# Optimization experiments

Hardware: AMD Instinct MI355X
Metric: run time of the kernel (lower is better)

The kernel has to match this reference:

```python
import jax, jax.numpy as jnp
import numpy as np


def setup_inputs() -> dict:
    key = jax.random.key(0)
    k1, k2, k3, k4 = jax.random.split(key, 4)
    batch, seq, d_model = 4, 4096, 2048
    num_atoms, num_layers, rank = 64, 16, 6
    hidden = jax.random.normal(k1, (batch, seq, d_model), dtype=jnp.float32)
    atom_scales = jax.random.uniform(k2, (batch, num_atoms), dtype=jnp.float32)
    # q_proj atoms: proj_dim == d_model == 2048
    A = jax.random.normal(k3, (num_atoms, num_layers, d_model, rank), dtype=jnp.float32) * 0.01
    B = jax.random.normal(k4, (num_atoms, num_layers, rank, d_model), dtype=jnp.float32) * 0.01
    return {"hidden": hidden, "atom_scales": atom_scales, "A": A, "B": B, "layer_idx": 5}


def reference(hidden, atom_scales, A, B, layer_idx):
    # Select this layer's atom factors: (atoms, d_model, rank) / (atoms, rank, proj_dim)
    A_l = A[:, layer_idx]
    B_l = B[:, layer_idx]
    # Down-project into rank-6 per atom: (batch, atoms, seq, rank)
    projections = jnp.einsum('bsd,adr->basr', hidden, A_l)
    # Per-(batch, atom) scalar blend weights
    scaled = projections * atom_scales[:, :, None, None]
    # Up-project and sum over atoms: (batch, seq, proj_dim)
    lora_out = jnp.einsum('basr,arp->bsp', scaled, B_l)
    return lora_out
```

## Files before the change

kernel.cpp:

```cpp
#include <hip/hip_runtime.h>
#include <hip/hip_bf16.h>

typedef __attribute__((ext_vector_type(4))) float  f32x4;
typedef __attribute__((ext_vector_type(8))) short  s16x8;

#define D_MODEL 2048
#define SEQ     4096
#define BATCH   4
#define NATOMS  64
#define RANK    6
#define NLAYERS 16
#define NAR     (NATOMS*RANK)
#define M_TOTAL (BATCH*SEQ)

#define ASZ  (64*72)
#define WSZ  (384*64)
#define BSZ  (64*392)
#define PSTR 392

static __device__ __forceinline__ unsigned short f2bf(float x){
    union { float f; unsigned u; } v; v.f = x;
    unsigned r = (v.u + 0x7FFF + ((v.u >> 16) & 1)) >> 16;
    return (unsigned short)r;
}

static __device__ __forceinline__ void gload_lds16(const void* g, void* l) {
    __builtin_amdgcn_global_load_lds(
        (const __attribute__((address_space(1))) unsigned int*)g,
        (__attribute__((address_space(3))) unsigned int*)l, 16, 0, 0);
}

static __device__ __forceinline__ s16x8 cvt8(f32x4 lo, f32x4 hi) {
    union { s16x8 v; unsigned short s[8]; } u;
    u.s[0] = f2bf(lo.x); u.s[1] = f2bf(lo.y); u.s[2] = f2bf(lo.z); u.s[3] = f2bf(lo.w);
    u.s[4] = f2bf(hi.x); u.s[5] = f2bf(hi.y); u.s[6] = f2bf(hi.z); u.s[7] = f2bf(hi.w);
    return u.v;
}

__global__ void prep_kernel(const float* __restrict__ A,
                            const float* __restrict__ B,
                            const int*   __restrict__ layer_idx,
                            unsigned short* __restrict__ WbfT,
                            unsigned short* __restrict__ BbfT)
{
    const int l = layer_idx[0];
    int idx = blockIdx.x * 256 + threadIdx.x;
    const int total = NAR * D_MODEL;
    if (idx < total) {
        int n = idx / D_MODEL, d = idx % D_MODEL;
        int a = n / RANK, r = n % RANK;
        float v = A[((size_t)(a*NLAYERS + l) * D_MODEL + d) * RANK + r];
        WbfT[idx] = f2bf(v);
    } else {
        idx -= total;
        int p = idx / NAR, n = idx % NAR;
        int a = n / RANK, r = n % RANK;
        float v = B[((size_t)(a*NLAYERS + l) * RANK + r) * D_MODEL + p];
        BbfT[idx] = f2bf(v);
    }
}

__global__ __launch_bounds__(512, 1) void fused_lora(
    const float*          __restrict__ hidden,
    const float*          __restrict__ scales,
    const unsigned short* __restrict__ WbfT,
    const unsigned short* __restrict__ BbfT,
    float*                __restrict__ out)
{
    __shared__ __align__(16) char smem[150528];
    unsigned short* Af = (unsigned short*)smem;
    unsigned short* Wf = (unsigned short*)(smem + 18432);
    unsigned short* Pl = (unsigned short*)smem;
    unsigned short* Bt = (unsigned short*)(smem + 50176);

    const int m0   = blockIdx.x * 64;
    const int tid  = threadIdx.x;
    const int lane = tid & 63;
    const int w    = tid >> 6;
    const int wr   = w >> 2, wc = w & 3;

    const int rowA = tid >> 3;
    const int c8A  = tid & 7;
    const float* srcA = hidden + (size_t)(m0 + rowA) * D_MODEL + c8A * 8;

    const unsigned short* srcW[6];
    int ldsW[6];
    #pragma unroll
    for (int j = 0; j < 6; ++j) {
        int i = w * 6 + j;
        int r = i * 8 + (lane >> 3);
        int c = (lane & 7) ^ (r & 7);
        srcW[j] = WbfT + (size_t)r * D_MODEL + c * 8;
        ldsW[j] = i * 512;
    }

    f32x4 acc[2][6] = {};
    f32x4 ga[2], gb[2];

    ga[0] = *reinterpret_cast<const f32x4*>(srcA);
    ga[1] = *reinterpret_cast<const f32x4*>(srcA + 4);
    srcA += 64;
    {
        s16x8 s = cvt8(ga[0], ga[1]);
        *reinterpret_cast<s16x8*>(&Af[rowA * 72 + c8A * 8]) = s;
    }
    #pragma unroll
    for (int j = 0; j < 6; ++j) { gload_lds16(srcW[j], &Wf[ldsW[j]]); srcW[j] += 64; }
    __builtin_amdgcn_sched_barrier(0);
    gb[0] = *reinterpret_cast<const f32x4*>(srcA);
    gb[1] = *reinterpret_cast<const f32x4*>(srcA + 4);
    srcA += 64;
    asm volatile("s_waitcnt vmcnt(2) lgkmcnt(0)" ::: "memory");
    __builtin_amdgcn_s_barrier();

    auto body = [&](int t, f32x4 (&gI)[2], f32x4 (&gC)[2]) {
        const int buf = t & 1;
        if (t < 31) {
            #pragma unroll
            for (int j = 0; j < 6; ++j) {
                gload_lds16(srcW[j], &Wf[(buf ^ 1) * WSZ + ldsW[j]]);
                srcW[j] += 64;
            }
        }
        __builtin_amdgcn_sched_barrier(0);
        if (t < 30) {
            gI[0] = *reinterpret_cast<const f32x4*>(srcA);
            gI[1] = *reinterpret_cast<const f32x4*>(srcA + 4);
            srcA += 64;
        }
        const unsigned short* Ar = &Af[buf * ASZ];
        const unsigned short* Wr = &Wf[buf * WSZ];
        #pragma unroll
        for (int kk = 0; kk < 2; ++kk) {
            const int kch = kk * 4 + (lane >> 4);
            s16x8 bfr[6], afr[2];
            #pragma unroll
            for (int ni = 0; ni < 6; ++ni) {
                int br = wc * 96 + ni * 16 + (lane & 15);
                bfr[ni] = *reinterpret_cast<const s16x8*>(
                    &Wr[br * 64 + ((kch ^ (br & 7)) << 3)]);
            }
            #pragma unroll
            for (int mi = 0; mi < 2; ++mi) {
                int ar = wr * 32 + mi * 16 + (lane & 15);
                afr[mi] = *reinterpret_cast<const s16x8*>(
                    &Ar[ar * 72 + kk * 32 + (lane >> 4) * 8]);
            }
            #pragma unroll
            for (int mi = 0; mi < 2; ++mi)
                #pragma unroll
                for (int ni = 0; ni < 6; ++ni)
                    acc[mi][ni] = __builtin_amdgcn_mfma_f32_16x16x32_bf16(
                        afr[mi], bfr[ni], acc[mi][ni], 0, 0, 0);
        }
        if (t < 31) {
            s16x8 s = cvt8(gC[0], gC[1]);
            *reinterpret_cast<s16x8*>(&Af[(buf ^ 1) * ASZ + rowA * 72 + c8A * 8]) = s;
            if (t == 30) asm volatile("s_waitcnt vmcnt(0) lgkmcnt(0)" ::: "memory");
            else         asm volatile("s_waitcnt vmcnt(2) lgkmcnt(0)" ::: "memory");
            __builtin_amdgcn_s_barrier();
        }
    };
    for (int tt = 0; tt < 32; tt += 2) {
        body(tt,     ga, gb);
        body(tt + 1, gb, ga);
    }
    __syncthreads();

    const int b = m0 >> 12;
    #pragma unroll
    for (int ni = 0; ni < 6; ++ni) {
        int col  = wc * 96 + ni * 16 + (lane & 15);
        float sc = scales[b * NATOMS + col / RANK];
        #pragma unroll
        for (int mi = 0; mi < 2; ++mi) {
            #pragma unroll
            for (int r = 0; r < 4; ++r) {
                int row = wr * 32 + mi * 16 + (lane >> 4) * 4 + r;
                Pl[row * PSTR + col] = f2bf(acc[mi][ni][r] * sc);
            }
        }
    }
    __syncthreads();

    const int wr2 = w >> 2, wp = w & 3;
    const unsigned short* srcB[6];
    int dstB[6];
    #pragma unroll
    for (int j = 0; j < 6; ++j) {
        int g  = j * 512 + tid;
        int rB = g / 48, cB = g % 48;
        srcB[j] = BbfT + (size_t)rB * NAR + cB * 8;
        dstB[j] = rB * PSTR + cB * 8;
    }
    s16x8 pf[2][12];
    #pragma unroll
    for (int mi = 0; mi < 2; ++mi)
        #pragma unroll
        for (int ks = 0; ks < 12; ++ks)
            pf[mi][ks] = *reinterpret_cast<const s16x8*>(
                &Pl[(wr2 * 32 + mi * 16 + (lane & 15)) * PSTR + (ks * 4 + (lane >> 4)) * 8]);

    s16x8 gB[6];
    #pragma unroll
    for (int j = 0; j < 6; ++j) gB[j] = *reinterpret_cast<const s16x8*>(srcB[j]);
    #pragma unroll
    for (int j = 0; j < 6; ++j) *reinterpret_cast<s16x8*>(&Bt[dstB[j]]) = gB[j];
    asm volatile("s_waitcnt lgkmcnt(0)" ::: "memory");
    __builtin_amdgcn_s_barrier();

    for (int pt = 0; pt < 32; ++pt) {
        const int buf = pt & 1;
        if (pt < 31) {
            #pragma unroll
            for (int j = 0; j < 6; ++j)
                gB[j] = *reinterpret_cast<const s16x8*>(srcB[j] + (size_t)(pt + 1) * 64 * NAR);
        }
        f32x4 a2[2] = {};
        #pragma unroll
        for (int ks = 0; ks < 12; ++ks) {
            s16x8 bfr = *reinterpret_cast<const s16x8*>(
                &Bt[buf * BSZ + (wp * 16 + (lane & 15)) * PSTR + (ks * 4 + (lane >> 4)) * 8]);
            #pragma unroll
            for (int mi = 0; mi < 2; ++mi)
                a2[mi] = __builtin_amdgcn_mfma_f32_16x16x32_bf16(
                    pf[mi][ks], bfr, a2[mi], 0, 0, 0);
        }
        #pragma unroll
        for (int mi = 0; mi < 2; ++mi) {
            #pragma unroll
            for (int r = 0; r < 4; ++r) {
                int row = m0 + wr2 * 32 + mi * 16 + (lane >> 4) * 4 + r;
                int col = pt * 64 + wp * 16 + (lane & 15);
                out[(size_t)row * D_MODEL + col] = a2[mi][r];
            }
        }
        if (pt < 31) {
            #pragma unroll
            for (int j = 0; j < 6; ++j)
                *reinterpret_cast<s16x8*>(&Bt[(buf ^ 1) * BSZ + dstB[j]]) = gB[j];
            asm volatile("s_waitcnt lgkmcnt(0)" ::: "memory");
            __builtin_amdgcn_s_barrier();
        }
    }
}

extern "C" void kernel_launch(void* const* d_in, const int* in_sizes, int n_in,
                              void* d_out, int out_size, void* d_ws, size_t ws_size,
                              hipStream_t stream)
{
    const float* hidden    = (const float*)d_in[0];
    const float* scales    = (const float*)d_in[1];
    const float* A         = (const float*)d_in[2];
    const float* B         = (const float*)d_in[3];
    const int*   layer_idx = (const int*)d_in[4];
    float* out = (float*)d_out;

    unsigned short* WbfT = (unsigned short*)d_ws;
    unsigned short* BbfT = WbfT + (size_t)NAR * D_MODEL;

    prep_kernel<<<(2 * NAR * D_MODEL) / 256, 256, 0, stream>>>(A, B, layer_idx, WbfT, BbfT);
    fused_lora<<<M_TOTAL / 64, 512, 0, stream>>>(hidden, scales, WbfT, BbfT, out);
}
```

Before: 93.97 us.

## Load up-projection B fragments directly into registers instead of staging through LDS

The second GEMM phase no longer copies B tiles into a double-buffered LDS area behind barriers. Each wave now loads its own B fragments from global memory straight into registers, double-buffered in a ping-pong loop, and re-reads the P fragments from LDS every iteration instead of keeping them in registers. This drops the per-tile barriers and LDS writes and shrinks the shared memory allocation. The cost is redundant global loads of B across the two row-waves, which should mostly hit L2, plus more LDS reads for P.

```diff
diff --git a/kernel.cpp b/kernel.cpp
--- a/kernel.cpp
+++ b/kernel.cpp
@@ -15,7 +15,6 @@
 
 #define ASZ  (64*72)
 #define WSZ  (384*64)
-#define BSZ  (64*392)
 #define PSTR 392
 
 static __device__ __forceinline__ unsigned short f2bf(float x){
@@ -67,11 +66,10 @@
     const unsigned short* __restrict__ BbfT,
     float*                __restrict__ out)
 {
-    __shared__ __align__(16) char smem[150528];
+    __shared__ __align__(16) char smem[116736];
     unsigned short* Af = (unsigned short*)smem;
     unsigned short* Wf = (unsigned short*)(smem + 18432);
     unsigned short* Pl = (unsigned short*)smem;
-    unsigned short* Bt = (unsigned short*)(smem + 50176);
 
     const int m0   = blockIdx.x * 64;
     const int tid  = threadIdx.x;
@@ -184,47 +182,31 @@
     __syncthreads();
 
     const int wr2 = w >> 2, wp = w & 3;
-    const unsigned short* srcB[6];
-    int dstB[6];
-    #pragma unroll
-    for (int j = 0; j < 6; ++j) {
-        int g  = j * 512 + tid;
-        int rB = g / 48, cB = g % 48;
-        srcB[j] = BbfT + (size_t)rB * NAR + cB * 8;
-        dstB[j] = rB * PSTR + cB * 8;
-    }
-    s16x8 pf[2][12];
-    #pragma unroll
-    for (int mi = 0; mi < 2; ++mi)
-        #pragma unroll
-        for (int ks = 0; ks < 12; ++ks)
-            pf[mi][ks] = *reinterpret_cast<const s16x8*>(
-                &Pl[(wr2 * 32 + mi * 16 + (lane & 15)) * PSTR + (ks * 4 + (lane >> 4)) * 8]);
-
-    s16x8 gB[6];
-    #pragma unroll
-    for (int j = 0; j < 6; ++j) gB[j] = *reinterpret_cast<const s16x8*>(srcB[j]);
-    #pragma unroll
-    for (int j = 0; j < 6; ++j) *reinterpret_cast<s16x8*>(&Bt[dstB[j]]) = gB[j];
-    asm volatile("s_waitcnt lgkmcnt(0)" ::: "memory");
-    __builtin_amdgcn_s_barrier();
-
-    for (int pt = 0; pt < 32; ++pt) {
-        const int buf = pt & 1;
+    const unsigned short* srcB2 =
+        BbfT + (size_t)(wp * 16 + (lane & 15)) * NAR + (lane >> 4) * 8;
+    const unsigned short* PlBase = &Pl[(wr2 * 32 + (lane & 15)) * PSTR + (lane >> 4) * 8];
+
+    s16x8 bA[12], bB[12];
+    #pragma unroll
+    for (int ks = 0; ks < 12; ++ks)
+        bA[ks] = *reinterpret_cast<const s16x8*>(srcB2 + ks * 32);
+
+    auto p2body = [&](int pt, s16x8 (&bC)[12], s16x8 (&bN)[12]) {
         if (pt < 31) {
-            #pragma unroll
-            for (int j = 0; j < 6; ++j)
-                gB[j] = *reinterpret_cast<const s16x8*>(srcB[j] + (size_t)(pt + 1) * 64 * NAR);
+            const unsigned short* s2 = srcB2 + (size_t)(pt + 1) * 64 * NAR;
+            #pragma unroll
+            for (int ks = 0; ks < 12; ++ks)
+                bN[ks] = *reinterpret_cast<const s16x8*>(s2 + ks * 32);
         }
         f32x4 a2[2] = {};
         #pragma unroll
         for (int ks = 0; ks < 12; ++ks) {
-            s16x8 bfr = *reinterpret_cast<const s16x8*>(
-                &Bt[buf * BSZ + (wp * 16 + (lane & 15)) * PSTR + (ks * 4 + (lane >> 4)) * 8]);
-            #pragma unroll
-            for (int mi = 0; mi < 2; ++mi)
+            #pragma unroll
+            for (int mi = 0; mi < 2; ++mi) {
+                s16x8 pfr = *reinterpret_cast<const s16x8*>(PlBase + mi * 16 * PSTR + ks * 32);
                 a2[mi] = __builtin_amdgcn_mfma_f32_16x16x32_bf16(
-                    pf[mi][ks], bfr, a2[mi], 0, 0, 0);
+                    pfr, bC[ks], a2[mi], 0, 0, 0);
+            }
         }
         #pragma unroll
         for (int mi = 0; mi < 2; ++mi) {
@@ -235,13 +217,10 @@
                 out[(size_t)row * D_MODEL + col] = a2[mi][r];
             }
         }
-        if (pt < 31) {
-            #pragma unroll
-            for (int j = 0; j < 6; ++j)
-                *reinterpret_cast<s16x8*>(&Bt[(buf ^ 1) * BSZ + dstB[j]]) = gB[j];
-            asm volatile("s_waitcnt lgkmcnt(0)" ::: "memory");
-            __builtin_amdgcn_s_barrier();
-        }
+    };
+    for (int pt = 0; pt < 32; pt += 2) {
+        p2body(pt,     bA, bB);
+        p2body(pt + 1, bB, bA);
     }
 }
 
```

Measured after the change: 146.8 us. +56.3%, slower.

## Shrink fused LoRA block to 32 rows and 256 threads for two blocks per CU

Applied to the files above, without the earlier changes.

Each block of the fused LoRA kernel now covers 32 rows with 4 waves instead of 64 rows with 8 waves. The smaller LDS footprint lets two blocks fit on one CU. The down-projection K step drops to 32 with a new XOR swizzle. The up-projection now streams B tiles through LDS with global_load_lds, split into two half-K buffers, instead of staging them through registers. The aim is better latency hiding through occupancy. The cost is that the weight tiles are read from L2 twice as often across blocks, and there are more barriers per tile.

```diff
diff --git a/kernel.cpp b/kernel.cpp
--- a/kernel.cpp
+++ b/kernel.cpp
@@ -3,20 +3,19 @@
 
 typedef __attribute__((ext_vector_type(4))) float  f32x4;
 typedef __attribute__((ext_vector_type(8))) short  s16x8;
+typedef __attribute__((ext_vector_type(4))) unsigned short u16x4;
 
 #define D_MODEL 2048
-#define SEQ     4096
-#define BATCH   4
 #define NATOMS  64
 #define RANK    6
 #define NLAYERS 16
-#define NAR     (NATOMS*RANK)
-#define M_TOTAL (BATCH*SEQ)
-
-#define ASZ  (64*72)
-#define WSZ  (384*64)
-#define BSZ  (64*392)
+#define NAR     384
+#define M_TOTAL 16384
+
+#define AFSZ 1280
+#define WFSZ 12288
 #define PSTR 392
+#define BTSZ 12288
 
 static __device__ __forceinline__ unsigned short f2bf(float x){
     union { float f; unsigned u; } v; v.f = x;
@@ -30,11 +29,10 @@
         (__attribute__((address_space(3))) unsigned int*)l, 16, 0, 0);
 }
 
-static __device__ __forceinline__ s16x8 cvt8(f32x4 lo, f32x4 hi) {
-    union { s16x8 v; unsigned short s[8]; } u;
-    u.s[0] = f2bf(lo.x); u.s[1] = f2bf(lo.y); u.s[2] = f2bf(lo.z); u.s[3] = f2bf(lo.w);
-    u.s[4] = f2bf(hi.x); u.s[5] = f2bf(hi.y); u.s[6] = f2bf(hi.z); u.s[7] = f2bf(hi.w);
-    return u.v;
+static __device__ __forceinline__ u16x4 cvt4(f32x4 v) {
+    u16x4 w;
+    w.x = f2bf(v.x); w.y = f2bf(v.y); w.z = f2bf(v.z); w.w = f2bf(v.w);
+    return w;
 }
 
 __global__ void prep_kernel(const float* __restrict__ A,
@@ -60,187 +58,168 @@
     }
 }
 
-__global__ __launch_bounds__(512, 1) void fused_lora(
+__global__ __launch_bounds__(256, 2) void fused_lora(
     const float*          __restrict__ hidden,
     const float*          __restrict__ scales,
     const unsigned short* __restrict__ WbfT,
     const unsigned short* __restrict__ BbfT,
     float*                __restrict__ out)
 {
-    __shared__ __align__(16) char smem[150528];
+    __shared__ __align__(16) char smem[74240];
     unsigned short* Af = (unsigned short*)smem;
-    unsigned short* Wf = (unsigned short*)(smem + 18432);
+    unsigned short* Wf = (unsigned short*)(smem + 5120);
     unsigned short* Pl = (unsigned short*)smem;
-    unsigned short* Bt = (unsigned short*)(smem + 50176);
-
-    const int m0   = blockIdx.x * 64;
+    unsigned short* Bt = (unsigned short*)(smem + 25088);
+
+    const int m0   = blockIdx.x * 32;
     const int tid  = threadIdx.x;
     const int lane = tid & 63;
     const int w    = tid >> 6;
-    const int wr   = w >> 2, wc = w & 3;
+    const int kq   = lane >> 4;
 
     const int rowA = tid >> 3;
-    const int c8A  = tid & 7;
-    const float* srcA = hidden + (size_t)(m0 + rowA) * D_MODEL + c8A * 8;
+    const int cA   = (tid & 7) * 4;
+    const float* srcA = hidden + (size_t)(m0 + rowA) * D_MODEL + cA;
 
     const unsigned short* srcW[6];
     int ldsW[6];
     #pragma unroll
     for (int j = 0; j < 6; ++j) {
         int i = w * 6 + j;
-        int r = i * 8 + (lane >> 3);
-        int c = (lane & 7) ^ (r & 7);
-        srcW[j] = WbfT + (size_t)r * D_MODEL + c * 8;
+        int g = i * 64 + lane;
+        int r = g >> 2, c = g & 3;
+        srcW[j] = WbfT + (size_t)r * D_MODEL + (c ^ ((r >> 1) & 3)) * 8;
         ldsW[j] = i * 512;
     }
 
     f32x4 acc[2][6] = {};
-    f32x4 ga[2], gb[2];
-
-    ga[0] = *reinterpret_cast<const f32x4*>(srcA);
-    ga[1] = *reinterpret_cast<const f32x4*>(srcA + 4);
-    srcA += 64;
-    {
-        s16x8 s = cvt8(ga[0], ga[1]);
-        *reinterpret_cast<s16x8*>(&Af[rowA * 72 + c8A * 8]) = s;
-    }
-    #pragma unroll
-    for (int j = 0; j < 6; ++j) { gload_lds16(srcW[j], &Wf[ldsW[j]]); srcW[j] += 64; }
-    __builtin_amdgcn_sched_barrier(0);
-    gb[0] = *reinterpret_cast<const f32x4*>(srcA);
-    gb[1] = *reinterpret_cast<const f32x4*>(srcA + 4);
-    srcA += 64;
-    asm volatile("s_waitcnt vmcnt(2) lgkmcnt(0)" ::: "memory");
-    __builtin_amdgcn_s_barrier();
-
-    auto body = [&](int t, f32x4 (&gI)[2], f32x4 (&gC)[2]) {
+    f32x4 g;
+
+    g = *reinterpret_cast<const f32x4*>(srcA); srcA += 32;
+    *reinterpret_cast<u16x4*>(&Af[rowA * 40 + cA]) = cvt4(g);
+    #pragma unroll
+    for (int j = 0; j < 6; ++j) { gload_lds16(srcW[j], &Wf[ldsW[j]]); srcW[j] += 32; }
+    __syncthreads();
+
+    for (int t = 0; t < 64; ++t) {
         const int buf = t & 1;
-        if (t < 31) {
+        if (t < 63) {
             #pragma unroll
             for (int j = 0; j < 6; ++j) {
-                gload_lds16(srcW[j], &Wf[(buf ^ 1) * WSZ + ldsW[j]]);
-                srcW[j] += 64;
-            }
-        }
-        __builtin_amdgcn_sched_barrier(0);
-        if (t < 30) {
-            gI[0] = *reinterpret_cast<const f32x4*>(srcA);
-            gI[1] = *reinterpret_cast<const f32x4*>(srcA + 4);
-            srcA += 64;
-        }
-        const unsigned short* Ar = &Af[buf * ASZ];
-        const unsigned short* Wr = &Wf[buf * WSZ];
-        #pragma unroll
-        for (int kk = 0; kk < 2; ++kk) {
-            const int kch = kk * 4 + (lane >> 4);
-            s16x8 bfr[6], afr[2];
-            #pragma unroll
-            for (int ni = 0; ni < 6; ++ni) {
-                int br = wc * 96 + ni * 16 + (lane & 15);
-                bfr[ni] = *reinterpret_cast<const s16x8*>(
-                    &Wr[br * 64 + ((kch ^ (br & 7)) << 3)]);
+                gload_lds16(srcW[j], &Wf[(buf ^ 1) * WFSZ + ldsW[j]]);
+                srcW[j] += 32;
+            }
+            g = *reinterpret_cast<const f32x4*>(srcA); srcA += 32;
+        }
+        const unsigned short* Ar = &Af[buf * AFSZ];
+        const unsigned short* Wr = &Wf[buf * WFSZ];
+        s16x8 bfr[6], afr[2];
+        #pragma unroll
+        for (int ni = 0; ni < 6; ++ni) {
+            int br = w * 96 + ni * 16 + (lane & 15);
+            bfr[ni] = *reinterpret_cast<const s16x8*>(
+                &Wr[br * 32 + ((kq ^ ((br >> 1) & 3)) << 3)]);
+        }
+        #pragma unroll
+        for (int mi = 0; mi < 2; ++mi)
+            afr[mi] = *reinterpret_cast<const s16x8*>(
+                &Ar[(mi * 16 + (lane & 15)) * 40 + kq * 8]);
+        #pragma unroll
+        for (int mi = 0; mi < 2; ++mi)
+            #pragma unroll
+            for (int ni = 0; ni < 6; ++ni)
+                acc[mi][ni] = __builtin_amdgcn_mfma_f32_16x16x32_bf16(
+                    afr[mi], bfr[ni], acc[mi][ni], 0, 0, 0);
+        if (t < 63) {
+            *reinterpret_cast<u16x4*>(&Af[(buf ^ 1) * AFSZ + rowA * 40 + cA]) = cvt4(g);
+            __syncthreads();
+        }
+    }
+    __syncthreads();
+
+    const int b = m0 >> 12;
+    #pragma unroll
+    for (int ni = 0; ni < 6; ++ni) {
+        int col  = w * 96 + ni * 16 + (lane & 15);
+        float sc = scales[b * NATOMS + col / RANK];
+        #pragma unroll
+        for (int mi = 0; mi < 2; ++mi) {
+            #pragma unroll
+            for (int r = 0; r < 4; ++r) {
+                int row = mi * 16 + kq * 4 + r;
+                Pl[row * PSTR + col] = f2bf(acc[mi][ni][r] * sc);
+            }
+        }
+    }
+    __syncthreads();
+
+    s16x8 pf[2][12];
+    #pragma unroll
+    for (int mi = 0; mi < 2; ++mi)
+        #pragma unroll
+        for (int ks = 0; ks < 12; ++ks) {
+            pf[mi][ks] = *reinterpret_cast<const s16x8*>(
+                &Pl[(mi * 16 + (lane & 15)) * PSTR + (ks * 4 + kq) * 8]);
+            asm volatile("" : "+v"(pf[mi][ks]));
+        }
+
+    const unsigned short* srcB[6];
+    int ldsB[6];
+    #pragma unroll
+    for (int j = 0; j < 6; ++j) {
+        int gi = (w * 6 + j) * 64 + lane;
+        int rr = gi / 24, cc = gi % 24;
+        srcB[j] = BbfT + (size_t)rr * NAR + (cc ^ (rr & 7)) * 8;
+        ldsB[j] = (w * 6 + j) * 512;
+    }
+    const int rB = w * 16 + (lane & 15);
+
+    #pragma unroll
+    for (int j = 0; j < 6; ++j) gload_lds16(srcB[j], &Bt[ldsB[j]]);
+    __syncthreads();
+
+    for (int tl = 0; tl < 32; ++tl) {
+        f32x4 a2[2] = {};
+        {
+            #pragma unroll
+            for (int j = 0; j < 6; ++j)
+                gload_lds16(srcB[j] + (size_t)tl * 64 * NAR + 192, &Bt[BTSZ + ldsB[j]]);
+            #pragma unroll
+            for (int ks = 0; ks < 6; ++ks) {
+                s16x8 bfr = *reinterpret_cast<const s16x8*>(
+                    &Bt[rB * 192 + (((ks * 4 + kq) ^ (rB & 7)) << 3)]);
+                #pragma unroll
+                for (int mi = 0; mi < 2; ++mi)
+                    a2[mi] = __builtin_amdgcn_mfma_f32_16x16x32_bf16(
+                        pf[mi][ks], bfr, a2[mi], 0, 0, 0);
+            }
+            __syncthreads();
+        }
+        {
+            if (tl < 31) {
+                #pragma unroll
+                for (int j = 0; j < 6; ++j)
+                    gload_lds16(srcB[j] + (size_t)(tl + 1) * 64 * NAR, &Bt[ldsB[j]]);
+            }
+            #pragma unroll
+            for (int ks = 0; ks < 6; ++ks) {
+                s16x8 bfr = *reinterpret_cast<const s16x8*>(
+                    &Bt[BTSZ + rB * 192 + (((ks * 4 + kq) ^ (rB & 7)) << 3)]);
+                #pragma unroll
+                for (int mi = 0; mi < 2; ++mi)
+                    a2[mi] = __builtin_amdgcn_mfma_f32_16x16x32_bf16(
+                        pf[mi][6 + ks], bfr, a2[mi], 0, 0, 0);
             }
             #pragma unroll
             for (int mi = 0; mi < 2; ++mi) {
-                int ar = wr * 32 + mi * 16 + (lane & 15);
-                afr[mi] = *reinterpret_cast<const s16x8*>(
-                    &Ar[ar * 72 + kk * 32 + (lane >> 4) * 8]);
-            }
-            #pragma unroll
-            for (int mi = 0; mi < 2; ++mi)
-                #pragma unroll
-                for (int ni = 0; ni < 6; ++ni)
-                    acc[mi][ni] = __builtin_amdgcn_mfma_f32_16x16x32_bf16(
-                        afr[mi], bfr[ni], acc[mi][ni], 0, 0, 0);
-        }
-        if (t < 31) {
-            s16x8 s = cvt8(gC[0], gC[1]);
-            *reinterpret_cast<s16x8*>(&Af[(buf ^ 1) * ASZ + rowA * 72 + c8A * 8]) = s;
-            if (t == 30) asm volatile("s_waitcnt vmcnt(0) lgkmcnt(0)" ::: "memory");
-            else         asm volatile("s_waitcnt vmcnt(2) lgkmcnt(0)" ::: "memory");
-            __builtin_amdgcn_s_barrier();
-        }
-    };
-    for (int tt = 0; tt < 32; tt += 2) {
-        body(tt,     ga, gb);
-        body(tt + 1, gb, ga);
-    }
-    __syncthreads();
-
-    const int b = m0 >> 12;
-    #pragma unroll
-    for (int ni = 0; ni < 6; ++ni) {
-        int col  = wc * 96 + ni * 16 + (lane & 15);
-        float sc = scales[b * NATOMS + col / RANK];
-        #pragma unroll
-        for (int mi = 0; mi < 2; ++mi) {
-            #pragma unroll
-            for (int r = 0; r < 4; ++r) {
-                int row = wr * 32 + mi * 16 + (lane >> 4) * 4 + r;
-                Pl[row * PSTR + col] = f2bf(acc[mi][ni][r] * sc);
-            }
-        }
-    }
-    __syncthreads();
-
-    const int wr2 = w >> 2, wp = w & 3;
-    const unsigned short* srcB[6];
-    int dstB[6];
-    #pragma unroll
-    for (int j = 0; j < 6; ++j) {
-        int g  = j * 512 + tid;
-        int rB = g / 48, cB = g % 48;
-        srcB[j] = BbfT + (size_t)rB * NAR + cB * 8;
-        dstB[j] = rB * PSTR + cB * 8;
-    }
-    s16x8 pf[2][12];
-    #pragma unroll
-    for (int mi = 0; mi < 2; ++mi)
-        #pragma unroll
-        for (int ks = 0; ks < 12; ++ks)
-            pf[mi][ks] = *reinterpret_cast<const s16x8*>(
-                &Pl[(wr2 * 32 + mi * 16 + (lane & 15)) * PSTR + (ks * 4 + (lane >> 4)) * 8]);
-
-    s16x8 gB[6];
-    #pragma unroll
-    for (int j = 0; j < 6; ++j) gB[j] = *reinterpret_cast<const s16x8*>(srcB[j]);
-    #pragma unroll
-    for (int j = 0; j < 6; ++j) *reinterpret_cast<s16x8*>(&Bt[dstB[j]]) = gB[j];
-    asm volatile("s_waitcnt lgkmcnt(0)" ::: "memory");
-    __builtin_amdgcn_s_barrier();
-
-    for (int pt = 0; pt < 32; ++pt) {
-        const int buf = pt & 1;
-        if (pt < 31) {
-            #pragma unroll
-            for (int j = 0; j < 6; ++j)
-                gB[j] = *reinterpret_cast<const s16x8*>(srcB[j] + (size_t)(pt + 1) * 64 * NAR);
-        }
-        f32x4 a2[2] = {};
-        #pragma unroll
-        for (int ks = 0; ks < 12; ++ks) {
-            s16x8 bfr = *reinterpret_cast<const s16x8*>(
-                &Bt[buf * BSZ + (wp * 16 + (lane & 15)) * PSTR + (ks * 4 + (lane >> 4)) * 8]);
-            #pragma unroll
-            for (int mi = 0; mi < 2; ++mi)
-                a2[mi] = __builtin_amdgcn_mfma_f32_16x16x32_bf16(
-                    pf[mi][ks], bfr, a2[mi], 0, 0, 0);
-        }
-        #pragma unroll
-        for (int mi = 0; mi < 2; ++mi) {
-            #pragma unroll
-            for (int r = 0; r < 4; ++r) {
-                int row = m0 + wr2 * 32 + mi * 16 + (lane >> 4) * 4 + r;
-                int col = pt * 64 + wp * 16 + (lane & 15);
-                out[(size_t)row * D_MODEL + col] = a2[mi][r];
-            }
-        }
-        if (pt < 31) {
-            #pragma unroll
-            for (int j = 0; j < 6; ++j)
-                *reinterpret_cast<s16x8*>(&Bt[(buf ^ 1) * BSZ + dstB[j]]) = gB[j];
-            asm volatile("s_waitcnt lgkmcnt(0)" ::: "memory");
-            __builtin_amdgcn_s_barrier();
+                #pragma unroll
+                for (int r = 0; r < 4; ++r) {
+                    int row = m0 + mi * 16 + kq * 4 + r;
+                    int col = tl * 64 + rB;
+                    out[(size_t)row * D_MODEL + col] = a2[mi][r];
+                }
+            }
+            if (tl < 31) __syncthreads();
         }
     }
 }
@@ -260,5 +239,5 @@
     unsigned short* BbfT = WbfT + (size_t)NAR * D_MODEL;
 
     prep_kernel<<<(2 * NAR * D_MODEL) / 256, 256, 0, stream>>>(A, B, layer_idx, WbfT, BbfT);
-    fused_lora<<<M_TOTAL / 64, 512, 0, stream>>>(hidden, scales, WbfT, BbfT, out);
-}
+    fused_lora<<<M_TOTAL / 32, 256, 0, stream>>>(hidden, scales, WbfT, BbfT, out);
+}
```

New measurement: 140.5 us. +49.6%, slower.
